# Kernel optimization log

Measured on AMD Instinct MI355X. Metric: run time of the kernel, lower is better.

## Reference

```python
import jax, jax.numpy as jnp
import numpy as np

EMBED_DIM = 1024
B, T = 4, 2048

def setup_inputs() -> dict:
    key = jax.random.key(0)
    ks = jax.random.split(key, 7)
    s = 1.0 / np.sqrt(EMBED_DIM)
    return {
        "x": jax.random.normal(ks[0], (B, T, EMBED_DIM), dtype=jnp.float32),
        "Wq": jax.random.uniform(ks[1], (EMBED_DIM, EMBED_DIM), jnp.float32, -s, s),
        "bq": jax.random.uniform(ks[2], (EMBED_DIM,), jnp.float32, -s, s),
        "Wk": jax.random.uniform(ks[3], (EMBED_DIM, EMBED_DIM), jnp.float32, -s, s),
        "bk": jax.random.uniform(ks[4], (EMBED_DIM,), jnp.float32, -s, s),
        "Wv": jax.random.uniform(ks[5], (EMBED_DIM, EMBED_DIM), jnp.float32, -s, s),
        "bv": jax.random.uniform(ks[6], (EMBED_DIM,), jnp.float32, -s, s),
    }

def reference(x, Wq, bq, Wk, bk, Wv, bv):
    Bsz, Tlen, C = x.shape
    # torch Linear: y = x @ W.T + b
    Q = jnp.einsum('btc,dc->btd', x, Wq) + bq
    K = jnp.einsum('btc,dc->btd', x, Wk) + bk
    V = jnp.einsum('btc,dc->btd', x, Wv) + bv
    score = jnp.einsum('bqd,bkd->bqk', Q, K) / jnp.sqrt(jnp.float32(C))
    causal = jnp.tril(jnp.ones((Tlen, Tlen), dtype=bool))  # [T,T]
    score = jnp.where(causal, score, -jnp.inf)
    att = jax.nn.softmax(score, axis=-1)
    return jnp.einsum('bqk,bkd->bqd', att, V)
```

## Files before the change

kernel.cpp:

```cpp
#include <hip/hip_runtime.h>


using u16 = unsigned short;
typedef __attribute__((ext_vector_type(8))) short short8;
typedef __attribute__((ext_vector_type(4))) float f32x4;

__device__ __forceinline__ u16 f2b(float f) {
  unsigned u = __builtin_bit_cast(unsigned, f);
  u += 0x7fffu + ((u >> 16) & 1u);
  return (u16)(u >> 16);
}

__device__ __forceinline__ float b2f(u16 h) {
  return __builtin_bit_cast(float, (unsigned)h << 16);
}

__device__ __forceinline__ void async16(void* lds, const void* g) {
  __builtin_amdgcn_global_load_lds(
      (const __attribute__((address_space(1))) unsigned int*)g,
      (__attribute__((address_space(3))) unsigned int*)lds, 16, 0, 0);
}

__device__ __forceinline__ void block_barrier() {
  asm volatile("" ::: "memory");
  __builtin_amdgcn_s_barrier();
  asm volatile("" ::: "memory");
}

__global__ __launch_bounds__(256) void cvt_all_kernel(
    const float* __restrict__ x, const float* __restrict__ Wq,
    const float* __restrict__ Wk, const float* __restrict__ Wv,
    u16* __restrict__ xb, u16* __restrict__ Wcat) {
  const int i = blockIdx.x * 256 + threadIdx.x;
  const float* src;
  u16* dst;
  int c;
  if (i < 2097152) {
    src = x; dst = xb; c = i;
  } else {
    const int r = i - 2097152;
    const int seg = r >> 18;
    src = seg == 0 ? Wq : (seg == 1 ? Wk : Wv);
    dst = Wcat + (size_t)seg * 1048576;
    c = r & 262143;
  }
  const float4 v = reinterpret_cast<const float4*>(src)[c];
  ushort4 o;
  o.x = f2b(v.x); o.y = f2b(v.y); o.z = f2b(v.z); o.w = f2b(v.w);
  reinterpret_cast<ushort4*>(dst)[c] = o;
}

#define STG_A(buf, half, roff, ku)                                          \
  {                                                                         \
    async16(&Asm[buf][half][tid * 8], gA0 + (size_t)(roff)*lda + (ku));     \
    async16(&Asm[buf][half][4096 + tid * 8],                                \
            gA0 + (size_t)((roff) + 128) * lda + (ku));                     \
  }
#define STG_B(buf, half, roff, ku)                                          \
  {                                                                         \
    async16(&Bsm[buf][half][tid * 8], gB0 + (size_t)(roff)*ldb + (ku));     \
    async16(&Bsm[buf][half][4096 + tid * 8],                                \
            gB0 + (size_t)((roff) + 128) * ldb + (ku));                     \
  }
#define RD_A(buf, hh)                                                       \
  {                                                                         \
    _Pragma("unroll") for (int ii = 0; ii < 4; ++ii) {                      \
      a[ii][0] = *(const short8*)(&Asm[buf][hh][aoff + ii * 1024 + sk0]);   \
      a[ii][1] = *(const short8*)(&Asm[buf][hh][aoff + ii * 1024 + sk1]);   \
    }                                                                       \
  }
#define RD_B(buf, cc, breg)                                                 \
  {                                                                         \
    _Pragma("unroll") for (int jj = 0; jj < 2; ++jj) {                      \
      breg[jj][0] = *(const short8*)(&Bsm[buf][cc][boff + jj * 1024 + sk0]);\
      breg[jj][1] = *(const short8*)(&Bsm[buf][cc][boff + jj * 1024 + sk1]);\
    }                                                                       \
  }
#define QUAD(hh, cc, breg)                                                  \
  {                                                                         \
    __builtin_amdgcn_s_setprio(1);                                          \
    _Pragma("unroll") for (int ii = 0; ii < 4; ++ii)                        \
        _Pragma("unroll") for (int jj = 0; jj < 2; ++jj) {                  \
      acc[(hh)*4 + ii][(cc)*2 + jj] =                                       \
          __builtin_amdgcn_mfma_f32_16x16x32_bf16(                          \
              a[ii][0], breg[jj][0], acc[(hh)*4 + ii][(cc)*2 + jj], 0,0,0); \
      acc[(hh)*4 + ii][(cc)*2 + jj] =                                       \
          __builtin_amdgcn_mfma_f32_16x16x32_bf16(                          \
              a[ii][1], breg[jj][1], acc[(hh)*4 + ii][(cc)*2 + jj], 0,0,0); \
    }                                                                       \
    __builtin_amdgcn_s_setprio(0);                                          \
  }
#define LGK0 asm volatile("s_waitcnt lgkmcnt(0)" ::: "memory")
#define VM6 asm volatile("s_waitcnt vmcnt(6)" ::: "memory")

template <int NT, typename Epi>
__device__ __forceinline__ void gemm256_8ph(const u16* __restrict__ A, int lda,
                                            const u16* __restrict__ B, int ldb,
                                            Epi&& epi) {
  __shared__ __align__(16) u16 Asm[2][2][8192];
  __shared__ __align__(16) u16 Bsm[2][2][8192];
  const int tid = threadIdx.x;
  const int lane = tid & 63;
  const int w = tid >> 6;
  const int wm = w >> 2;
  const int wn = w & 3;

  f32x4 acc[8][4];
#pragma unroll
  for (int i = 0; i < 8; ++i)
#pragma unroll
    for (int j = 0; j < 4; ++j) acc[i][j] = f32x4{0.f, 0.f, 0.f, 0.f};

  const int sr = tid >> 3;
  const int ce = ((tid & 7) ^ (sr & 7)) << 3;
  const u16* gA0 = A + (size_t)sr * lda + ce;
  const int bE = (sr & 31) + ((sr >> 5) << 6);
  const u16* gB0 = B + (size_t)bE * ldb + ce;

  const int l15 = lane & 15;
  const int hi = lane >> 4;
  const int lo7 = lane & 7;
  const int aoff = wm * 4096 + l15 * 64;
  const int boff = wn * 2048 + l15 * 64;
  const int sk0 = (hi ^ lo7) << 3;
  const int sk1 = ((4 + hi) ^ lo7) << 3;

  short8 a[4][2], bEr[2][2], bLr[2][2];

  STG_A(0, 0, 0, 0); STG_B(0, 0, 0, 0); STG_A(0, 1, 64, 0); STG_B(0, 1, 32, 0);
  STG_A(1, 0, 0, 64); STG_B(1, 0, 0, 64); STG_A(1, 1, 64, 64);
  VM6;
  block_barrier();

  for (int t = 0; t < NT; t += 2) {
    const int k1 = (t + 1) * 64;
    const int t2c = (t + 2 < NT) ? (t + 2) : (NT - 1);
    const int t3c = (t + 3 < NT) ? (t + 3) : (NT - 1);
    const int k2 = t2c * 64;
    const int k3 = t3c * 64;
    RD_A(0, 0); RD_B(0, 0, bEr); STG_B(1, 1, 32, k1);
    block_barrier(); LGK0; QUAD(0, 0, bEr); block_barrier();
    RD_B(0, 1, bLr); STG_A(0, 0, 0, k2);
    block_barrier(); LGK0; QUAD(0, 1, bLr); block_barrier();
    RD_A(0, 1); STG_B(0, 0, 0, k2);
    block_barrier(); LGK0; QUAD(1, 1, bLr); block_barrier();
    STG_A(0, 1, 64, k2);
    VM6; block_barrier(); QUAD(1, 0, bEr); block_barrier();
    RD_A(1, 0); RD_B(1, 0, bEr); STG_B(0, 1, 32, k2);
    block_barrier(); LGK0; QUAD(0, 0, bEr); block_barrier();
    RD_B(1, 1, bLr); STG_A(1, 0, 0, k3);
    block_barrier(); LGK0; QUAD(0, 1, bLr); block_barrier();
    RD_A(1, 1); STG_B(1, 0, 0, k3);
    block_barrier(); LGK0; QUAD(1, 1, bLr); block_barrier();
    STG_A(1, 1, 64, k3);
    VM6; block_barrier(); QUAD(1, 0, bEr); block_barrier();
  }
  asm volatile("s_waitcnt vmcnt(0)" ::: "memory");
  epi(acc, wm, wn, lane);
}

__global__ __launch_bounds__(512, 1) void qkv_qk_kernel(
    const u16* __restrict__ xb, const u16* __restrict__ Wcat,
    const float* __restrict__ bq, const float* __restrict__ bk,
    u16* __restrict__ Qb, u16* __restrict__ Kb) {
  const int bid = blockIdx.x;
  const int swz = (bid & 7) * 32 + (bid >> 3);
  const int mt = swz >> 3, nt = swz & 7;
  const int z = nt >> 2;
  const float* bias = z ? bk : bq;
  u16* out = z ? Kb : Qb;
  const float scale = z ? 1.0f : 0.03125f;
  gemm256_8ph<16>(
      xb + (size_t)mt * 256 * 1024, 1024, Wcat + (size_t)nt * 256 * 1024, 1024,
      [&](f32x4(&acc)[8][4], int wm, int wn, int lane) {
        const int r0 = mt * 256 + wm * 128 + ((lane >> 4) << 2);
        const int c0 = (nt & 3) * 256 + wn * 64 + (lane & 15);
#pragma unroll
        for (int i8 = 0; i8 < 8; ++i8) {
          const int rb = r0 + (i8 >> 2) * 64 + (i8 & 3) * 16;
#pragma unroll
          for (int i4 = 0; i4 < 4; ++i4) {
            const int col = c0 + (i4 >> 1) * 32 + (i4 & 1) * 16;
            const float bb = bias[col];
#pragma unroll
            for (int rr = 0; rr < 4; ++rr)
              out[(size_t)(rb + rr) * 1024 + col] =
                  f2b((acc[i8][i4][rr] + bb) * scale);
          }
        }
      });
}

template <typename Epi>
__device__ __forceinline__ void gemm_bt_tile(const u16* __restrict__ A, int lda,
                                             const u16* __restrict__ B, int ldb,
                                             int nt, Epi&& epi) {
  __shared__ __align__(16) u16 As[128 * 64];
  __shared__ __align__(16) u16 Bs[128 * 64];
  const int tid = threadIdx.x;
  const int lane = tid & 63;
  const int w = tid >> 6;
  const int wr = (w >> 1) << 6;
  const int wc = (w & 1) << 6;

  f32x4 acc[4][4];
#pragma unroll
  for (int i = 0; i < 4; ++i)
#pragma unroll
    for (int j = 0; j < 4; ++j) acc[i][j] = f32x4{0.f, 0.f, 0.f, 0.f};

  const int sr = tid >> 3;
  const int ce = ((tid & 7) ^ (sr & 7)) << 3;
  const u16* gA = A + (size_t)sr * lda + ce;
  const u16* gB = B + (size_t)sr * ldb + ce;
  u16* const dA = As + tid * 8;
  u16* const dB = Bs + tid * 8;

  const int hi = lane >> 4;
  const int lo7 = lane & 7;
  const int ra = (wr + (lane & 15)) << 6;
  const int rb = (wc + (lane & 15)) << 6;
  const int sk0 = (hi ^ lo7) << 3;
  const int sk1 = ((4 + hi) ^ lo7) << 3;

  for (int t = 0; t < nt; ++t) {
    __syncthreads();
#pragma unroll
    for (int s = 0; s < 4; ++s) {
      async16(dA + s * 2048, gA + (size_t)(s * 32) * lda);
      async16(dB + s * 2048, gB + (size_t)(s * 32) * ldb);
    }
    gA += 64;
    gB += 64;
    __syncthreads();
#pragma unroll
    for (int kk = 0; kk < 2; ++kk) {
      const int sk = kk ? sk1 : sk0;
      short8 af[4], bf[4];
#pragma unroll
      for (int i = 0; i < 4; ++i)
        af[i] = *(const short8*)(As + ra + i * 1024 + sk);
#pragma unroll
      for (int j = 0; j < 4; ++j)
        bf[j] = *(const short8*)(Bs + rb + j * 1024 + sk);
#pragma unroll
      for (int i = 0; i < 4; ++i)
#pragma unroll
        for (int j = 0; j < 4; ++j)
          acc[i][j] = __builtin_amdgcn_mfma_f32_16x16x32_bf16(af[i], bf[j],
                                                              acc[i][j], 0, 0, 0);
    }
  }
  epi(acc, wr, wc, lane);
}

template <typename Epi>
__device__ __forceinline__ void gemm_bt_128k(const u16* __restrict__ A, int lda,
                                             const u16* __restrict__ B, int ldb,
                                             int nt, Epi&& epi) {
  __shared__ __align__(16) u16 As[2][128 * 64];
  __shared__ __align__(16) u16 Bs[2][128 * 64];
  const int tid = threadIdx.x;
  const int lane = tid & 63;
  const int w = tid >> 6;
  const int wr = (w >> 1) << 6;
  const int wc = (w & 1) << 6;

  f32x4 acc[4][4];
#pragma unroll
  for (int i = 0; i < 4; ++i)
#pragma unroll
    for (int j = 0; j < 4; ++j) acc[i][j] = f32x4{0.f, 0.f, 0.f, 0.f};

  const int sr = tid >> 3;
  const int ce = ((tid & 7) ^ (sr & 7)) << 3;
  const u16* gA = A + (size_t)sr * lda + ce;
  const u16* gB = B + (size_t)sr * ldb + ce;

  const int hi = lane >> 4;
  const int lo7 = lane & 7;
  const int ra = (wr + (lane & 15)) << 6;
  const int rb = (wc + (lane & 15)) << 6;
  const int sk0 = (hi ^ lo7) << 3;
  const int sk1 = ((4 + hi) ^ lo7) << 3;

  for (int t = 0; t < nt; ++t) {
    __syncthreads();
#pragma unroll
    for (int kh = 0; kh < 2; ++kh)
#pragma unroll
      for (int s = 0; s < 4; ++s) {
        async16(&As[kh][tid * 8 + s * 2048],
                gA + kh * 64 + (size_t)(s * 32) * lda);
        async16(&Bs[kh][tid * 8 + s * 2048],
                gB + kh * 64 + (size_t)(s * 32) * ldb);
      }
    gA += 128;
    gB += 128;
    __syncthreads();
#pragma unroll
    for (int kk = 0; kk < 4; ++kk) {
      const int kh = kk >> 1;
      const int sk = (kk & 1) ? sk1 : sk0;
      short8 af[4], bf[4];
#pragma unroll
      for (int i = 0; i < 4; ++i)
        af[i] = *(const short8*)(&As[kh][ra + i * 1024 + sk]);
#pragma unroll
      for (int j = 0; j < 4; ++j)
        bf[j] = *(const short8*)(&Bs[kh][rb + j * 1024 + sk]);
#pragma unroll
      for (int i = 0; i < 4; ++i)
#pragma unroll
        for (int j = 0; j < 4; ++j)
          acc[i][j] = __builtin_amdgcn_mfma_f32_16x16x32_bf16(af[i], bf[j],
                                                              acc[i][j], 0, 0, 0);
    }
  }
  epi(acc, wr, wc, lane);
}

__global__ __launch_bounds__(256) void qkv_v_kernel(
    const u16* __restrict__ xb, const u16* __restrict__ Wcat,
    const float* __restrict__ bv, u16* __restrict__ Vtb) {
  const int bid = blockIdx.x;
  const int u = bid >> 3;
  const int nt = (bid & 7) * 8 + (u >> 3);
  const int mt = u & 7;
  const u16* Wvb = Wcat + (size_t)2 * 1048576;
  gemm_bt_tile(
      Wvb + (size_t)mt * 128 * 1024, 1024, xb + (size_t)nt * 128 * 1024, 1024, 16,
      [&](f32x4(&acc)[4][4], int wr, int wc, int lane) {
        const int r0 = mt * 128 + wr + ((lane >> 4) << 2);
        const int c0 = nt * 128 + wc + (lane & 15);
#pragma unroll
        for (int i = 0; i < 4; ++i)
#pragma unroll
          for (int rr = 0; rr < 4; ++rr) {
            const int row = r0 + i * 16 + rr;
            const float bb = bv[row];
#pragma unroll
            for (int j = 0; j < 4; ++j)
              Vtb[(size_t)row * 8192 + c0 + j * 16] = f2b(acc[i][j][rr] + bb);
          }
      });
}

__global__ __launch_bounds__(256) void score_kernel(const u16* __restrict__ Qb,
                                                    const u16* __restrict__ Kb,
                                                    u16* __restrict__ S) {
  const int b = blockIdx.y;
  const int traw = blockIdx.x;
  const int t = (traw & 7) * 17 + (traw >> 3);
  int qt = 0;
  while ((qt + 1) * (qt + 2) / 2 <= t) ++qt;
  const int kt = t - (qt * (qt + 1)) / 2;
  const u16* A = Qb + ((size_t)b * 2048 + qt * 128) * 1024;
  const u16* Bp = Kb + ((size_t)b * 2048 + kt * 128) * 1024;
  u16* Sb = S + (size_t)b * 2048 * 2048;
  gemm_bt_tile(A, 1024, Bp, 1024, 16,
               [&](f32x4(&acc)[4][4], int wr, int wc, int lane) {
                 const int r0 = qt * 128 + wr + ((lane >> 4) << 2);
                 const int c0 = kt * 128 + wc + (lane & 15);
#pragma unroll
                 for (int i = 0; i < 4; ++i)
#pragma unroll
                   for (int j = 0; j < 4; ++j)
#pragma unroll
                     for (int rr = 0; rr < 4; ++rr)
                       Sb[(size_t)(r0 + i * 16 + rr) * 2048 + c0 + j * 16] =
                           f2b(acc[i][j][rr]);
               });
}

__global__ __launch_bounds__(256) void softmax_kernel(const u16* __restrict__ S,
                                                      u16* __restrict__ P) {
  __shared__ float redm[4], reds[4];
  const int rowid = blockIdx.x;
  const int b = rowid >> 11;
  const int q = rowid & 2047;
  const u16* Srow = S + ((size_t)b * 2048 + q) * 2048;
  u16* Prow = P + ((size_t)b * 2048 + q) * 2048;
  const int L = q + 1;
  const int Lpad = ((q >> 7) + 1) << 7;
  const int tid = threadIdx.x;
  const int k0 = tid << 3;
  const bool active = k0 < Lpad;
  float v[8];
  float m = -1e30f;
  if (active) {
    const short8 s8 = *(const short8*)(Srow + k0);
#pragma unroll
    for (int j = 0; j < 8; ++j) {
      v[j] = (k0 + j < L) ? b2f((u16)s8[j]) : -1e30f;
      m = fmaxf(m, v[j]);
    }
  }
#pragma unroll
  for (int o = 32; o > 0; o >>= 1) m = fmaxf(m, __shfl_xor(m, o));
  if ((tid & 63) == 0) redm[tid >> 6] = m;
  __syncthreads();
  m = fmaxf(fmaxf(redm[0], redm[1]), fmaxf(redm[2], redm[3]));
  float s = 0.f;
  if (active) {
#pragma unroll
    for (int j = 0; j < 8; ++j) {
      const float e = (k0 + j < L) ? __expf(v[j] - m) : 0.f;
      v[j] = e;
      s += e;
    }
  }
#pragma unroll
  for (int o = 32; o > 0; o >>= 1) s += __shfl_xor(s, o);
  if ((tid & 63) == 0) reds[tid >> 6] = s;
  __syncthreads();
  s = reds[0] + reds[1] + reds[2] + reds[3];
  const float inv = 1.0f / s;
  if (active) {
    short8 o8;
#pragma unroll
    for (int j = 0; j < 8; ++j)
      o8[j] = (short)((k0 + j < L) ? f2b(v[j] * inv) : (u16)0);
    *(short8*)(Prow + k0) = o8;
  }
}

__global__ __launch_bounds__(256) void pv_kernel(const u16* __restrict__ P,
                                                 const u16* __restrict__ Vtb,
                                                 float* __restrict__ O) {
  const int bid = blockIdx.x;
  const int g = bid >> 5;
  const int qt = (g & 1) ? ((g - 1) >> 1) : (15 - (g >> 1));
  const int inner = bid & 31;
  const int b = inner >> 3;
  const int dt = inner & 7;
  const u16* A = P + (size_t)b * 2048 * 2048 + (size_t)qt * 128 * 2048;
  const u16* Bp = Vtb + (size_t)dt * 128 * 8192 + b * 2048;
  float* Ob = O + (size_t)b * 2048 * 1024;
  gemm_bt_128k(A, 2048, Bp, 8192, qt + 1,
               [&](f32x4(&acc)[4][4], int wr, int wc, int lane) {
                 const int r0 = qt * 128 + wr + ((lane >> 4) << 2);
                 const int c0 = dt * 128 + wc + (lane & 15);
#pragma unroll
                 for (int i = 0; i < 4; ++i)
#pragma unroll
                   for (int j = 0; j < 4; ++j)
#pragma unroll
                     for (int rr = 0; rr < 4; ++rr)
                       Ob[(size_t)(r0 + i * 16 + rr) * 1024 + c0 + j * 16] =
                           acc[i][j][rr];
               });
}

extern "C" void kernel_launch(void* const* d_in, const int* in_sizes, int n_in,
                              void* d_out, int out_size, void* d_ws, size_t ws_size,
                              hipStream_t stream) {
  const float* x = (const float*)d_in[0];
  const float* Wq = (const float*)d_in[1];
  const float* bq = (const float*)d_in[2];
  const float* Wk = (const float*)d_in[3];
  const float* bk = (const float*)d_in[4];
  const float* Wv = (const float*)d_in[5];
  const float* bv = (const float*)d_in[6];
  float* out = (float*)d_out;
  char* ws = (char*)d_ws;
  u16* Qb = (u16*)(ws);
  u16* Kb = (u16*)(ws + (16u << 20));
  u16* Vtb = (u16*)(ws + (32u << 20));
  u16* xb = (u16*)(ws + (48u << 20));
  u16* Wcat = (u16*)(ws + (64u << 20));
  u16* S = (u16*)(ws + (70u << 20));
  u16* P = (u16*)(ws + (134u << 20));

  cvt_all_kernel<<<11264, 256, 0, stream>>>(x, Wq, Wk, Wv, xb, Wcat);
  qkv_qk_kernel<<<256, 512, 0, stream>>>(xb, Wcat, bq, bk, Qb, Kb);
  qkv_v_kernel<<<512, 256, 0, stream>>>(xb, Wcat, bv, Vtb);
  score_kernel<<<dim3(136, 4), 256, 0, stream>>>(Qb, Kb, S);
  softmax_kernel<<<8192, 256, 0, stream>>>(S, P);
  pv_kernel<<<512, 256, 0, stream>>>(P, Vtb, out);
}
```

Baseline: 149.3 us.

## Use 256x256 eight-phase GEMM for causal score tiles and add partial LDS wait

Replaces the 128x128 score kernel with a 512-thread kernel that reuses the 256x256 eight-phase pipelined GEMM already used for the Q/K projection. Causal lower-triangular tiles are enumerated at the 256 granularity, giving 144 blocks, with an XCD-aware block swizzle. A partial lgkmcnt(8) wait is also inserted before the first barrier of each half-iteration in the shared GEMM loop. Larger tiles improve operand reuse and use the tuned pipeline. The cost is more wasted work on diagonal tiles and fewer blocks than CUs, which can leave the machine underfilled.

```diff
diff --git a/kernel.cpp b/kernel.cpp
--- a/kernel.cpp
+++ b/kernel.cpp
@@ -91,6 +91,7 @@
     __builtin_amdgcn_s_setprio(0);                                          \
   }
 #define LGK0 asm volatile("s_waitcnt lgkmcnt(0)" ::: "memory")
+#define LGK8 asm volatile("s_waitcnt lgkmcnt(8)" ::: "memory")
 #define VM6 asm volatile("s_waitcnt vmcnt(6)" ::: "memory")
 
 template <int NT, typename Epi>
@@ -138,7 +139,7 @@
     const int t3c = (t + 3 < NT) ? (t + 3) : (NT - 1);
     const int k2 = t2c * 64;
     const int k3 = t3c * 64;
-    RD_A(0, 0); RD_B(0, 0, bEr); STG_B(1, 1, 32, k1);
+    RD_A(0, 0); RD_B(0, 0, bEr); STG_B(1, 1, 32, k1); LGK8;
     block_barrier(); LGK0; QUAD(0, 0, bEr); block_barrier();
     RD_B(0, 1, bLr); STG_A(0, 0, 0, k2);
     block_barrier(); LGK0; QUAD(0, 1, bLr); block_barrier();
@@ -146,7 +147,7 @@
     block_barrier(); LGK0; QUAD(1, 1, bLr); block_barrier();
     STG_A(0, 1, 64, k2);
     VM6; block_barrier(); QUAD(1, 0, bEr); block_barrier();
-    RD_A(1, 0); RD_B(1, 0, bEr); STG_B(0, 1, 32, k2);
+    RD_A(1, 0); RD_B(1, 0, bEr); STG_B(0, 1, 32, k2); LGK8;
     block_barrier(); LGK0; QUAD(0, 0, bEr); block_barrier();
     RD_B(1, 1, bLr); STG_A(1, 0, 0, k3);
     block_barrier(); LGK0; QUAD(0, 1, bLr); block_barrier();
@@ -191,6 +192,37 @@
       });
 }
 
+__global__ __launch_bounds__(512, 1) void score256_kernel(
+    const u16* __restrict__ Qb, const u16* __restrict__ Kb,
+    u16* __restrict__ S) {
+  const int bid = blockIdx.x;
+  const int t = (bid & 7) * 18 + (bid >> 3);
+  const int b = t / 36;
+  const int r = t % 36;
+  int qt = 0;
+  while ((qt + 1) * (qt + 2) / 2 <= r) ++qt;
+  const int kt = r - qt * (qt + 1) / 2;
+  u16* Sb = S + (size_t)b * 2048 * 2048;
+  gemm256_8ph<16>(
+      Qb + ((size_t)b * 2048 + qt * 256) * 1024, 1024,
+      Kb + ((size_t)b * 2048 + kt * 256) * 1024, 1024,
+      [&](f32x4(&acc)[8][4], int wm, int wn, int lane) {
+        const int r0 = qt * 256 + wm * 128 + ((lane >> 4) << 2);
+        const int c0 = kt * 256 + wn * 64 + (lane & 15);
+#pragma unroll
+        for (int i8 = 0; i8 < 8; ++i8) {
+          const int rb = r0 + (i8 >> 2) * 64 + (i8 & 3) * 16;
+#pragma unroll
+          for (int i4 = 0; i4 < 4; ++i4) {
+            const int col = c0 + (i4 >> 1) * 32 + (i4 & 1) * 16;
+#pragma unroll
+            for (int rr = 0; rr < 4; ++rr)
+              Sb[(size_t)(rb + rr) * 2048 + col] = f2b(acc[i8][i4][rr]);
+          }
+        }
+      });
+}
+
 template <typename Epi>
 __device__ __forceinline__ void gemm_bt_tile(const u16* __restrict__ A, int lda,
                                              const u16* __restrict__ B, int ldb,
@@ -344,33 +376,6 @@
               Vtb[(size_t)row * 8192 + c0 + j * 16] = f2b(acc[i][j][rr] + bb);
           }
       });
-}
-
-__global__ __launch_bounds__(256) void score_kernel(const u16* __restrict__ Qb,
-                                                    const u16* __restrict__ Kb,
-                                                    u16* __restrict__ S) {
-  const int b = blockIdx.y;
-  const int traw = blockIdx.x;
-  const int t = (traw & 7) * 17 + (traw >> 3);
-  int qt = 0;
-  while ((qt + 1) * (qt + 2) / 2 <= t) ++qt;
-  const int kt = t - (qt * (qt + 1)) / 2;
-  const u16* A = Qb + ((size_t)b * 2048 + qt * 128) * 1024;
-  const u16* Bp = Kb + ((size_t)b * 2048 + kt * 128) * 1024;
-  u16* Sb = S + (size_t)b * 2048 * 2048;
-  gemm_bt_tile(A, 1024, Bp, 1024, 16,
-               [&](f32x4(&acc)[4][4], int wr, int wc, int lane) {
-                 const int r0 = qt * 128 + wr + ((lane >> 4) << 2);
-                 const int c0 = kt * 128 + wc + (lane & 15);
-#pragma unroll
-                 for (int i = 0; i < 4; ++i)
-#pragma unroll
-                   for (int j = 0; j < 4; ++j)
-#pragma unroll
-                     for (int rr = 0; rr < 4; ++rr)
-                       Sb[(size_t)(r0 + i * 16 + rr) * 2048 + c0 + j * 16] =
-                           f2b(acc[i][j][rr]);
-               });
 }
 
 __global__ __launch_bounds__(256) void softmax_kernel(const u16* __restrict__ S,
@@ -475,7 +480,7 @@
   cvt_all_kernel<<<11264, 256, 0, stream>>>(x, Wq, Wk, Wv, xb, Wcat);
   qkv_qk_kernel<<<256, 512, 0, stream>>>(xb, Wcat, bq, bk, Qb, Kb);
   qkv_v_kernel<<<512, 256, 0, stream>>>(xb, Wcat, bv, Vtb);
-  score_kernel<<<dim3(136, 4), 256, 0, stream>>>(Qb, Kb, S);
+  score256_kernel<<<144, 512, 0, stream>>>(Qb, Kb, S);
   softmax_kernel<<<8192, 256, 0, stream>>>(S, P);
   pv_kernel<<<512, 256, 0, stream>>>(P, Vtb, out);
 }
```

New measurement: 151.7 us. No clear change (+1.6%).
